# Optimization experiments

Hardware: AMD Instinct MI355X
Metric: run time of the kernel (lower is better)

## Reference

```python
import jax, jax.numpy as jnp
import numpy as np

IN_FEATURES = 128
OUT_FEATURES = 1
N_NODES = 100000
N_EDGES = 640000


def setup_inputs() -> dict:
    key = jax.random.key(0)
    k1, k2, k3, k4, k5 = jax.random.split(key, 5)
    inp = jax.random.normal(k1, (N_NODES, IN_FEATURES), dtype=jnp.float32)
    edge_src = jax.random.randint(k2, (N_EDGES,), 0, N_NODES, dtype=jnp.int64)
    edge_trg = jax.random.randint(k3, (N_EDGES,), 0, N_NODES, dtype=jnp.int64)
    # Linear(2*in_features, out_features) with xavier_uniform weight init
    fan_in, fan_out = 2 * IN_FEATURES, OUT_FEATURES
    limit = float(np.sqrt(6.0 / (fan_in + fan_out)))
    W = jax.random.uniform(k4, (OUT_FEATURES, 2 * IN_FEATURES), dtype=jnp.float32,
                           minval=-limit, maxval=limit)
    b_lim = 1.0 / float(np.sqrt(fan_in))
    b = jax.random.uniform(k5, (OUT_FEATURES,), dtype=jnp.float32,
                           minval=-b_lim, maxval=b_lim)
    return {"input": inp, "edge_src_nodes": edge_src, "edge_trg_nodes": edge_trg,
            "W": W, "b": b}


def reference(input, W, b, edge_src_nodes, edge_trg_nodes):
    x = input.reshape(-1, input.shape[-1])          # [N, d]
    src = x[edge_src_nodes]                         # [E, d] gather
    trg = x[edge_trg_nodes]                         # [E, d] gather
    # Linear on concat(src, trg) == src @ W_src^T + trg @ W_trg^T (avoids concat materialization)
    d = x.shape[-1]
    W_src, W_trg = W[:, :d], W[:, d:]
    logits = src @ W_src.T + trg @ W_trg.T + b      # [E, out_features]
    return jax.nn.sigmoid(logits)
```

## Files before the change

kernel.cpp:

```cpp
#include <hip/hip_runtime.h>
#include <hip/hip_bf16.h>

#define N_FEAT 128

__global__ __launch_bounds__(256) void project_kernel(
    const float* __restrict__ x, const float* __restrict__ W,
    float* __restrict__ p_src, float* __restrict__ p_trg, int n_nodes)
{
    int gid  = blockIdx.x * blockDim.x + threadIdx.x;
    int node = gid >> 5;
    int sub  = threadIdx.x & 31;
    if (node >= n_nodes) return;

    const float4 xv = *reinterpret_cast<const float4*>(x + (size_t)node * N_FEAT + 4 * sub);
    const float4 ws = *reinterpret_cast<const float4*>(W + 4 * sub);
    const float4 wt = *reinterpret_cast<const float4*>(W + N_FEAT + 4 * sub);

    float ssrc = fmaf(xv.x, ws.x, fmaf(xv.y, ws.y, fmaf(xv.z, ws.z, xv.w * ws.w)));
    float strg = fmaf(xv.x, wt.x, fmaf(xv.y, wt.y, fmaf(xv.z, wt.z, xv.w * wt.w)));

    #pragma unroll
    for (int off = 16; off > 0; off >>= 1) {
        ssrc += __shfl_down(ssrc, off, 32);
        strg += __shfl_down(strg, off, 32);
    }
    if (sub == 0) {
        p_src[node] = ssrc;
        p_trg[node] = strg;
    }
}

__global__ __launch_bounds__(256) void edge_kernel(
    const int* __restrict__ esrc, const int* __restrict__ etrg,
    const float* __restrict__ p_src, const float* __restrict__ p_trg,
    const float* __restrict__ b, float* __restrict__ out, int n_edges4)
{
    int i = blockIdx.x * blockDim.x + threadIdx.x;
    if (i >= n_edges4) return;
    const int4 s = reinterpret_cast<const int4*>(esrc)[i];
    const int4 t = reinterpret_cast<const int4*>(etrg)[i];
    const float bias = b[0];

    float4 o;
    o.x = 1.0f / (1.0f + __expf(-(p_src[s.x] + p_trg[t.x] + bias)));
    o.y = 1.0f / (1.0f + __expf(-(p_src[s.y] + p_trg[t.y] + bias)));
    o.z = 1.0f / (1.0f + __expf(-(p_src[s.z] + p_trg[t.z] + bias)));
    o.w = 1.0f / (1.0f + __expf(-(p_src[s.w] + p_trg[t.w] + bias)));
    reinterpret_cast<float4*>(out)[i] = o;
}

extern "C" void kernel_launch(void* const* d_in, const int* in_sizes, int n_in,
                              void* d_out, int out_size, void* d_ws, size_t ws_size,
                              hipStream_t stream)
{
    const float* x    = (const float*)d_in[0];
    const int*   esrc = (const int*)d_in[1];
    const int*   etrg = (const int*)d_in[2];
    const float* W    = (const float*)d_in[3];
    const float* b    = (const float*)d_in[4];
    float* out = (float*)d_out;

    int n_nodes = in_sizes[0] / N_FEAT;
    int n_edges = in_sizes[1];

    float* p_src = (float*)d_ws;
    float* p_trg = p_src + n_nodes;

    const int threads = 256;
    int blocks1 = (n_nodes * 32 + threads - 1) / threads;
    project_kernel<<<blocks1, threads, 0, stream>>>(x, W, p_src, p_trg, n_nodes);

    int n_edges4 = n_edges / 4;
    int blocks2 = (n_edges4 + threads - 1) / threads;
    edge_kernel<<<blocks2, threads, 0, stream>>>(esrc, etrg, p_src, p_trg, b, out, n_edges4);
}
```

Before: 99.11 us.

## Fuse projection and edge kernels into one cooperative persistent kernel with grid sync

```diff
diff --git a/kernel.cpp b/kernel.cpp
--- a/kernel.cpp
+++ b/kernel.cpp
@@ -1,7 +1,68 @@
 #include <hip/hip_runtime.h>
-#include <hip/hip_bf16.h>
+#include <hip/hip_cooperative_groups.h>
+
+namespace cg = cooperative_groups;
 
 #define N_FEAT 128
+#define NBLK   1024
+#define NTHR   256
+#define NSEG   ((NBLK * NTHR) / 32)
+
+__global__ __launch_bounds__(NTHR, 4) void fused_kernel(
+    const float* __restrict__ x, const float* __restrict__ W,
+    const float* __restrict__ b,
+    const int* __restrict__ esrc, const int* __restrict__ etrg,
+    float* __restrict__ out, float* __restrict__ p_src, float* __restrict__ p_trg,
+    int n_nodes, int n_edges4)
+{
+    const int tid = blockIdx.x * NTHR + threadIdx.x;
+    const int sub = threadIdx.x & 31;
+    const int seg = tid >> 5;
+
+    const float4 wsv = *reinterpret_cast<const float4*>(W + 4 * sub);
+    const float4 wtv = *reinterpret_cast<const float4*>(W + N_FEAT + 4 * sub);
+
+    int node = seg;
+    if (node < n_nodes) {
+        float4 xv = *reinterpret_cast<const float4*>(x + (size_t)node * N_FEAT + 4 * sub);
+        for (;;) {
+            const int nxt = node + NSEG;
+            const bool more = (nxt < n_nodes);
+            float4 xn;
+            if (more)
+                xn = *reinterpret_cast<const float4*>(x + (size_t)nxt * N_FEAT + 4 * sub);
+
+            float ssrc = fmaf(xv.x, wsv.x, fmaf(xv.y, wsv.y, fmaf(xv.z, wsv.z, xv.w * wsv.w)));
+            float strg = fmaf(xv.x, wtv.x, fmaf(xv.y, wtv.y, fmaf(xv.z, wtv.z, xv.w * wtv.w)));
+            #pragma unroll
+            for (int off = 16; off > 0; off >>= 1) {
+                ssrc += __shfl_down(ssrc, off, 32);
+                strg += __shfl_down(strg, off, 32);
+            }
+            if (sub == 0) {
+                p_src[node] = ssrc;
+                p_trg[node] = strg;
+            }
+            if (!more) break;
+            node = nxt;
+            xv = xn;
+        }
+    }
+
+    cg::this_grid().sync();
+
+    const float bias = b[0];
+    for (int i = tid; i < n_edges4; i += NBLK * NTHR) {
+        const int4 s = reinterpret_cast<const int4*>(esrc)[i];
+        const int4 t = reinterpret_cast<const int4*>(etrg)[i];
+        float4 o;
+        o.x = 1.0f / (1.0f + __expf(-(p_src[s.x] + p_trg[t.x] + bias)));
+        o.y = 1.0f / (1.0f + __expf(-(p_src[s.y] + p_trg[t.y] + bias)));
+        o.z = 1.0f / (1.0f + __expf(-(p_src[s.z] + p_trg[t.z] + bias)));
+        o.w = 1.0f / (1.0f + __expf(-(p_src[s.w] + p_trg[t.w] + bias)));
+        reinterpret_cast<float4*>(out)[i] = o;
+    }
+}
 
 __global__ __launch_bounds__(256) void project_kernel(
     const float* __restrict__ x, const float* __restrict__ W,
@@ -60,17 +121,24 @@
     const float* b    = (const float*)d_in[4];
     float* out = (float*)d_out;
 
-    int n_nodes = in_sizes[0] / N_FEAT;
-    int n_edges = in_sizes[1];
+    int n_nodes  = in_sizes[0] / N_FEAT;
+    int n_edges  = in_sizes[1];
+    int n_edges4 = n_edges / 4;
 
     float* p_src = (float*)d_ws;
     float* p_trg = p_src + n_nodes;
 
-    const int threads = 256;
-    int blocks1 = (n_nodes * 32 + threads - 1) / threads;
-    project_kernel<<<blocks1, threads, 0, stream>>>(x, W, p_src, p_trg, n_nodes);
-
-    int n_edges4 = n_edges / 4;
-    int blocks2 = (n_edges4 + threads - 1) / threads;
-    edge_kernel<<<blocks2, threads, 0, stream>>>(esrc, etrg, p_src, p_trg, b, out, n_edges4);
+    void* args[] = { (void*)&x, (void*)&W, (void*)&b, (void*)&esrc, (void*)&etrg,
+                     (void*)&out, (void*)&p_src, (void*)&p_trg,
+                     (void*)&n_nodes, (void*)&n_edges4 };
+    hipError_t err = hipLaunchCooperativeKernel((void*)fused_kernel,
+                                                dim3(NBLK), dim3(NTHR),
+                                                args, 0, stream);
+    if (err != hipSuccess) {
+        const int threads = 256;
+        int blocks1 = (n_nodes * 32 + threads - 1) / threads;
+        project_kernel<<<blocks1, threads, 0, stream>>>(x, W, p_src, p_trg, n_nodes);
+        int blocks2 = (n_edges4 + threads - 1) / threads;
+        edge_kernel<<<blocks2, threads, 0, stream>>>(esrc, etrg, p_src, p_trg, b, out, n_edges4);
+    }
 }
```

After: 202.0 us. 2.04x slower.
